# Kernel tuning notes

Hardware: AMD Instinct MI355X
Metric: run time of the kernel (lower is better)

The kernel has to match this reference:

```python
import jax, jax.numpy as jnp
import numpy as np

B, T, HID = 1, 2048, 1024
H, D = 16, 64
S = 64            # selection_block_size / sliding window / compress block
MAXK = 8          # max_selected_blocks
W_ENT, W_SP = 0.01, 0.01
NB = T // S       # 32 blocks (T divisible by S -> no padding branch)


def setup_inputs() -> dict:
    key = jax.random.key(0)
    ks = jax.random.split(key, 8)
    rn = lambda k, shp, s=0.02: jax.random.normal(k, shp, jnp.float32) * s
    return {
        'hidden_states': rn(ks[0], (B, T, HID), 1.0),
        'Wq': rn(ks[1], (HID, H * D)),
        'Wk': rn(ks[2], (HID, H * D)),
        'Wv': rn(ks[3], (HID, H * D)),
        'Wo': rn(ks[4], (H * D, HID)),
        'Wc': rn(ks[5], (S * D, D)),      # shared k/v compress MLP (same module in torch)
        'bc': jnp.zeros((D,), jnp.float32),
        'k_scale': jnp.ones((1,), jnp.float32),
        'k_bias': jnp.zeros((1,), jnp.float32),
        'Ws': rn(ks[6], (HID, 3 * H)),
        'bs': jnp.zeros((3 * H,), jnp.float32),
    }


def _local_attn(q, k, v):
    # lucidrains LocalAttention: window S, causal, look_backward=1, scale d^-0.5
    b, h, t, d = q.shape
    nw = t // S
    qw = q.reshape(b, h, nw, S, d)
    kw = k.reshape(b, h, nw, S, d)
    vw = v.reshape(b, h, nw, S, d)
    k_prev = jnp.concatenate([jnp.zeros_like(kw[:, :, :1]), kw[:, :, :-1]], axis=2)
    v_prev = jnp.concatenate([jnp.zeros_like(vw[:, :, :1]), vw[:, :, :-1]], axis=2)
    kc = jnp.concatenate([k_prev, kw], axis=3)   # (b,h,nw,2S,d)
    vc = jnp.concatenate([v_prev, vw], axis=3)
    scores = jnp.einsum('bhwid,bhwjd->bhwij', qw, kc) / jnp.sqrt(jnp.float32(d))
    qpos = jnp.arange(S)[:, None]
    krel = jnp.arange(2 * S)[None, :] - S        # key pos relative to window start
    wins = jnp.arange(nw)[:, None, None]
    allowed = (krel <= qpos)[None] & (wins * S + krel[None] >= 0)  # (nw,S,2S)
    NEG = -jnp.finfo(scores.dtype).max
    scores = jnp.where(allowed[None, None], scores, NEG)
    p = jax.nn.softmax(scores, axis=-1)
    return jnp.einsum('bhwij,bhwjd->bhwid', p, vc).reshape(b, h, t, d)


def reference(hidden_states, Wq, Wk, Wv, Wo, Wc, bc, k_scale, k_bias, Ws, bs):
    x = hidden_states
    scale = 1.0 / jnp.sqrt(jnp.float32(D))
    q = (x @ Wq).reshape(B, T, H, D).transpose(0, 2, 1, 3)
    k = (x @ Wk).reshape(B, T, H, D).transpose(0, 2, 1, 3)
    v = (x @ Wv).reshape(B, T, H, D).transpose(0, 2, 1, 3)

    sliding_out = _local_attn(q, k, v)

    # block compression (shared MLP for k and v, exact-erf GELU as in torch)
    k_blk = k.reshape(B, H, NB, S * D)
    v_blk = v.reshape(B, H, NB, S * D)
    kc = jax.nn.gelu(k_blk @ Wc + bc, approximate=False)   # (B,H,NB,D)
    vc = jax.nn.gelu(v_blk @ Wc + bc, approximate=False)

    importance = jnp.einsum('bhid,bhjd->bhij', q, kc) * scale   # (B,H,T,NB)
    comp_probs = jax.nn.softmax(importance, axis=-1)
    comp_out = jnp.einsum('bhij,bhjd->bhid', comp_probs, vc)

    # per-query-block scores, entropy-driven dynamic k
    block_scores = importance.reshape(B, H, NB, S, NB).mean(axis=3)   # (B,H,NB,NB)
    block_probs = jax.nn.softmax(block_scores, axis=-1)
    entropy = -jnp.sum(block_probs * jnp.log(block_probs + 1e-9), axis=-1)
    max_entropy = jnp.log(jnp.float32(NB))
    norm_ent = entropy / (max_entropy + 1e-9)
    k_ratio = jax.nn.sigmoid(k_scale[0] * norm_ent + k_bias[0])
    dynamic_k = jnp.clip(MAXK * k_ratio, 1.0, float(MAXK)).astype(jnp.int32)  # torch .long() truncates
    avg_k = dynamic_k.astype(jnp.float32).mean()

    _, topk_idx = jax.lax.top_k(block_scores, MAXK)                 # (B,H,NB,MAXK)
    k_mask = jnp.arange(MAXK)[None, None, None, :] < dynamic_k[..., None]
    sel = (topk_idx[..., None] == jnp.arange(NB)) & k_mask[..., None]
    mask = sel.any(axis=-2)                                         # (B,H,NB,NB)
    mask = mask | jnp.eye(NB, dtype=bool)[None, None]
    sparse_mask = jnp.repeat(jnp.repeat(mask, S, axis=2), S, axis=3)  # (B,H,T,T)

    attn = jnp.einsum('bhid,bhjd->bhij', q, k) * scale
    NEG = -jnp.finfo(attn.dtype).max
    attn = jnp.where(sparse_mask, attn, NEG)
    fine_probs = jax.nn.softmax(attn, axis=-1)
    fine_out = jnp.einsum('bhij,bhjd->bhid', fine_probs, v)

    strategy = jax.nn.sigmoid(x @ Ws + bs).reshape(B, T, H, 3).transpose(0, 2, 1, 3)  # (B,H,T,3)
    combined = jnp.stack([sliding_out, comp_out, fine_out], axis=-1)  # (B,H,T,D,3)
    out = jnp.einsum('bhnds,bhns->bhnd', combined, strategy)
    merged = out.transpose(0, 2, 1, 3).reshape(B, T, H * D)
    output = merged @ Wo

    entropy_loss = jnp.mean((k_ratio - norm_ent) ** 2)
    aux_loss = W_ENT * entropy_loss + W_SP * k_ratio.mean()
    return output, avg_k, aux_loss
```

## Files before the change

### kernel.cpp

```cpp
#include <hip/hip_runtime.h>
#include <math.h>
#include <stdint.h>

typedef unsigned short u16;
typedef short v8s __attribute__((ext_vector_type(8)));
typedef float v4f __attribute__((ext_vector_type(4)));

constexpr int kT   = 2048;
constexpr int kHID = 1024;
constexpr int kH   = 16;
constexpr int kNB  = 32;
constexpr size_t MB = 1ull << 20;

__device__ __forceinline__ float b2f(u16 u) { unsigned x = ((unsigned)u) << 16; return __uint_as_float(x); }
__device__ __forceinline__ u16 f2b(float f) {
  unsigned x = __float_as_uint(f);
  x += 0x7FFFu + ((x >> 16) & 1u);
  return (u16)(x >> 16);
}
__device__ __forceinline__ v4f mfma16(v8s a, v8s b, v4f c) {
  return __builtin_amdgcn_mfma_f32_16x16x32_bf16(a, b, c, 0, 0, 0);
}
__device__ __forceinline__ void gl_lds16(const void* g, void* l) {
  __builtin_amdgcn_global_load_lds((const __attribute__((address_space(1))) uint32_t*)g,
                                   (__attribute__((address_space(3))) uint32_t*)l, 16, 0, 0);
}

__global__ __launch_bounds__(256) void prep_kernel(
    const float* __restrict__ x, const float* __restrict__ Wq, const float* __restrict__ Wk,
    const float* __restrict__ Wv, const float* __restrict__ Wo, const float* __restrict__ Wc,
    const float* __restrict__ Wsp,
    u16* __restrict__ xh,
    u16* __restrict__ WqtH, u16* __restrict__ WktH,
    u16* __restrict__ WvtH, u16* __restrict__ WotH, u16* __restrict__ WctH, u16* __restrict__ WctL,
    u16* __restrict__ Wst) {
  __shared__ float tbuf[32][33];
  int bid = blockIdx.x;
  const int tid = threadIdx.x;
  if (bid < 1024) {
    int i = bid * 2048 + tid * 8;
    float4 a = *(const float4*)(x + i), b = *(const float4*)(x + i + 4);
    float tv[8] = {a.x, a.y, a.z, a.w, b.x, b.y, b.z, b.w};
    union { u16 s[8]; uint4 u; } hs;
#pragma unroll
    for (int e = 0; e < 8; ++e) hs.s[e] = f2b(tv[e]);
    *(uint4*)(xh + i) = hs.u;
    return;
  }
  bid -= 1024;
  const float* W; u16* Hh; u16* Ll; int Kd, Nd, bx, by;
  if (bid < 4096) {
    int wsel = bid >> 10, sub = bid & 1023;
    W  = wsel == 0 ? Wq : wsel == 1 ? Wk : wsel == 2 ? Wv : Wo;
    Hh = wsel == 0 ? WqtH : wsel == 1 ? WktH : wsel == 2 ? WvtH : WotH;
    Ll = nullptr;
    Kd = 1024; Nd = 1024;
    bx = (sub & 31) * 32; by = (sub >> 5) * 32;
  } else if (bid < 4096 + 256) {
    int sub = bid - 4096;
    W = Wc; Hh = WctH; Ll = WctL;
    Kd = 4096; Nd = 64;
    bx = (sub & 1) * 32; by = (sub >> 1) * 32;
  } else {
    int i = (bid - 4096 - 256) * 256 + tid;
    int n = i >> 10, k2 = i & 1023;
    float v = (n < 48) ? Wsp[(size_t)k2 * 48 + n] : 0.f;
    Wst[(size_t)n * 1024 + k2] = f2b(v);
    return;
  }
  const int lx = tid & 31, ly = tid >> 5;
  for (int i2 = ly; i2 < 32; i2 += 8) tbuf[i2][lx] = W[(size_t)(by + i2) * Nd + bx + lx];
  __syncthreads();
  for (int i2 = ly; i2 < 32; i2 += 8) {
    float xv = tbuf[lx][i2];
    size_t idx = (size_t)(bx + i2) * Kd + by + lx;
    u16 h = f2b(xv);
    Hh[idx] = h;
    if (Ll) Ll[idx] = f2b(xv - b2f(h));
  }
}

__global__ __launch_bounds__(256) void proj_gemm(const u16* __restrict__ xh,
                                                 const u16* __restrict__ WkH, const u16* __restrict__ WqH,
                                                 const u16* __restrict__ WvH, const u16* __restrict__ Wst,
                                                 const float* __restrict__ bsp,
                                                 u16* __restrict__ kbf, u16* __restrict__ qh,
                                                 u16* __restrict__ vbf, float* __restrict__ strat) {
  __shared__ u16 AsH[64 * 64], BsH[128 * 64];
  const int b = blockIdx.x;
  const int slot = (b & 7) * 100 + (b >> 3);
  const int panel = slot >> 5, bmi = slot & 31;
  int z, bni;
  if (panel < 8)       { z = 0; bni = panel; }
  else if (panel < 16) { z = 1; bni = panel - 8; }
  else if (panel < 24) { z = 2; bni = panel - 16; }
  else                 { z = 3; bni = 0; }
  const int bm = bmi * 64, bn = bni * 128;
  const u16* Bh = (z == 0) ? WkH : (z == 1) ? WqH : (z == 2) ? WvH : Wst;
  const int tid = threadIdx.x, w = tid >> 6, lane = tid & 63;
  const int lg = lane >> 4, l16 = lane & 15;
  const int wr = w >> 1, wc = w & 1;
  v4f acc[2][4] = {};
  for (int k0 = 0; k0 < kHID; k0 += 64) {
    __syncthreads();
#pragma unroll
    for (int p = 0; p < 2; ++p) {
      int s = tid + p * 256, row = s >> 3, sf = (s & 7) ^ (row & 7);
      gl_lds16(xh + (size_t)(bm + row) * kHID + k0 + sf * 8, (char*)AsH + s * 16);
    }
#pragma unroll
    for (int p = 0; p < 4; ++p) {
      int s = tid + p * 256, row = s >> 3, sf = (s & 7) ^ (row & 7);
      gl_lds16(Bh + (size_t)(bn + row) * kHID + k0 + sf * 8, (char*)BsH + s * 16);
    }
    __syncthreads();
#pragma unroll
    for (int kk = 0; kk < 2; ++kk) {
      v8s bh4[4];
#pragma unroll
      for (int j = 0; j < 4; ++j) {
        int col = wc * 64 + j * 16 + l16;
        bh4[j] = *(const v8s*)((const char*)BsH + col * 128 + (((kk * 4 + lg) ^ (col & 7)) * 16));
      }
#pragma unroll
      for (int i = 0; i < 2; ++i) {
        int row = wr * 32 + i * 16 + l16;
        v8s ah = *(const v8s*)((const char*)AsH + row * 128 + (((kk * 4 + lg) ^ (row & 7)) * 16));
#pragma unroll
        for (int j = 0; j < 4; ++j) acc[i][j] = mfma16(ah, bh4[j], acc[i][j]);
      }
    }
  }
#pragma unroll
  for (int i = 0; i < 2; ++i)
#pragma unroll
    for (int j = 0; j < 4; ++j)
#pragma unroll
      for (int r = 0; r < 4; ++r) {
        int row = bm + wr * 32 + i * 16 + lg * 4 + r;
        int col = bn + wc * 64 + j * 16 + l16;
        float val = acc[i][j][r];
        if (z == 3) {
          if (col < 48) strat[(size_t)row * 48 + col] = 1.f / (1.f + expf(-(val + bsp[col])));
        } else {
          u16 hh = f2b(val);
          size_t idx = (size_t)row * kHID + col;
          if (z == 0) kbf[idx] = hh;
          else if (z == 1) qh[idx] = hh;
          else vbf[idx] = hh;
        }
      }
}

__global__ __launch_bounds__(256) void cgemm_fused(const u16* __restrict__ kbf,
                                                   const u16* __restrict__ vbf,
                                                   const u16* __restrict__ WcH, const u16* __restrict__ WcL,
                                                   float* __restrict__ Pk, float* __restrict__ Pv) {
  __shared__ u16 AsH[64 * 64], BsH[64 * 64], BsL[64 * 64];
  const int bm = blockIdx.y * 64;
  const int isK = (blockIdx.z < 8);
  const int ks = isK ? blockIdx.z : blockIdx.z - 8;
  const u16* Asrc = isK ? kbf : vbf;
  float* P = isK ? Pk : Pv;
  const int tid = threadIdx.x;
  const int w = tid >> 6, lane = tid & 63;
  const int lg = lane >> 4, l16 = lane & 15;
  const int wr = w >> 1, wc = w & 1;
  v4f acc[2][2] = {};
  for (int k0 = ks * 512; k0 < ks * 512 + 512; k0 += 64) {
    __syncthreads();
#pragma unroll
    for (int ss = 0; ss < 2; ++ss) {
      int s = tid + ss * 256, row = s >> 3, sf = (s & 7) ^ (row & 7);
      int r = bm + row;
      size_t abase = ((size_t)((r & 31) * 64 + (k0 >> 6))) * kHID + (r >> 5) * 64 + sf * 8;
      gl_lds16(Asrc + abase, (char*)AsH + s * 16);
      gl_lds16(WcH + (size_t)row * 4096 + k0 + sf * 8, (char*)BsH + s * 16);
      if (isK) gl_lds16(WcL + (size_t)row * 4096 + k0 + sf * 8, (char*)BsL + s * 16);
    }
    __syncthreads();
    v8s ah[2][2], bh[2][2];
#pragma unroll
    for (int i = 0; i < 2; ++i)
#pragma unroll
      for (int kk = 0; kk < 2; ++kk) {
        int row = wr * 32 + i * 16 + l16;
        ah[i][kk] = *(const v8s*)((const char*)AsH + row * 128 + (((kk * 4 + lg) ^ (row & 7)) * 16));
        int col = wc * 32 + i * 16 + l16;
        bh[i][kk] = *(const v8s*)((const char*)BsH + col * 128 + (((kk * 4 + lg) ^ (col & 7)) * 16));
      }
#pragma unroll
    for (int i = 0; i < 2; ++i)
#pragma unroll
      for (int j = 0; j < 2; ++j) {
        acc[i][j] = mfma16(ah[i][0], bh[j][0], acc[i][j]);
        acc[i][j] = mfma16(ah[i][1], bh[j][1], acc[i][j]);
      }
    if (isK) {
      v8s bl[2][2];
#pragma unroll
      for (int i = 0; i < 2; ++i)
#pragma unroll
        for (int kk = 0; kk < 2; ++kk) {
          int col = wc * 32 + i * 16 + l16;
          bl[i][kk] = *(const v8s*)((const char*)BsL + col * 128 + (((kk * 4 + lg) ^ (col & 7)) * 16));
        }
#pragma unroll
      for (int i = 0; i < 2; ++i)
#pragma unroll
        for (int j = 0; j < 2; ++j) {
          acc[i][j] = mfma16(ah[i][0], bl[j][0], acc[i][j]);
          acc[i][j] = mfma16(ah[i][1], bl[j][1], acc[i][j]);
        }
    }
  }
#pragma unroll
  for (int i = 0; i < 2; ++i)
#pragma unroll
    for (int j = 0; j < 2; ++j)
#pragma unroll
      for (int r = 0; r < 4; ++r) {
        int row = bm + wr * 32 + i * 16 + lg * 4 + r;
        int col = wc * 32 + j * 16 + l16;
        P[(size_t)ks * 32768 + (size_t)row * 64 + col] = acc[i][j][r];
      }
}

__global__ __launch_bounds__(256) void impsel_mfma(const u16* __restrict__ qh,
                                                   const float* __restrict__ Pk,
                                                   const float* __restrict__ Pv,
                                                   const float* __restrict__ bc,
                                                   const float* __restrict__ strat,
                                                   const float* __restrict__ kscale_p,
                                                   const float* __restrict__ kbias_p,
                                                   unsigned* __restrict__ maskb,
                                                   float* __restrict__ krb,
                                                   float* __restrict__ neb,
                                                   int* __restrict__ dkb,
                                                   u16* __restrict__ merged) {
  __shared__ u16 KCH[32 * 64], KCL[32 * 64], VCT[64 * 32];
  __shared__ u16 Pl[4][16 * 32];
  __shared__ float red[4][32];
  const int tt = blockIdx.x, h = blockIdx.y;
  const int tid = threadIdx.x, w = tid >> 6, lane = tid & 63;
  const int lg = lane >> 4, l16 = lane & 15;
  {
    int nb = tid >> 3, seg = tid & 7;
    {
      const float* base = Pk + ((size_t)(h * 32 + nb) * 64 + seg * 8);
      float v[8] = {};
#pragma unroll
      for (int ks = 0; ks < 8; ++ks) {
        const float* p = base + (size_t)ks * 32768;
        float4 a = *(const float4*)p, bq = *(const float4*)(p + 4);
        v[0] += a.x; v[1] += a.y; v[2] += a.z; v[3] += a.w;
        v[4] += bq.x; v[5] += bq.y; v[6] += bq.z; v[7] += bq.w;
      }
      v8s hi, lo;
#pragma unroll
      for (int e = 0; e < 8; ++e) {
        float s = v[e] + bc[seg * 8 + e];
        float g = 0.5f * s * (1.f + erff(s * 0.70710678118654752f));
        u16 hh = f2b(g);
        hi[e] = (short)hh;
        lo[e] = (short)f2b(g - b2f(hh));
      }
      *(v8s*)((char*)KCH + nb * 128 + ((seg ^ (nb & 7)) * 16)) = hi;
      *(v8s*)((char*)KCL + nb * 128 + ((seg ^ (nb & 7)) * 16)) = lo;
    }
    {
      const float* base = Pv + ((size_t)(h * 32 + nb) * 64 + seg * 8);
      float v[8] = {};
#pragma unroll
      for (int ks = 0; ks < 8; ++ks) {
        const float* p = base + (size_t)ks * 32768;
        float4 a = *(const float4*)p, bq = *(const float4*)(p + 4);
        v[0] += a.x; v[1] += a.y; v[2] += a.z; v[3] += a.w;
        v[4] += bq.x; v[5] += bq.y; v[6] += bq.z; v[7] += bq.w;
      }
#pragma unroll
      for (int e = 0; e < 8; ++e) {
        int d = seg * 8 + e;
        float s = v[e] + bc[d];
        float g = 0.5f * s * (1.f + erff(s * 0.70710678118654752f));
        *((u16*)((char*)VCT + d * 64 + (((nb >> 3) ^ (d & 3)) * 16) + (nb & 7) * 2)) = f2b(g);
      }
    }
  }
  __syncthreads();
  const size_t qoff = (size_t)(tt * 64 + w * 16 + l16) * kHID + h * 64;
  v8s ah[2];
  ah[0] = *(const v8s*)(qh + qoff + lg * 8);
  ah[1] = *(const v8s*)(qh + qoff + 32 + lg * 8);
  v4f sa[2] = {};
#pragma unroll
  for (int ct = 0; ct < 2; ++ct) {
    int col = ct * 16 + l16;
#pragma unroll
    for (int kk = 0; kk < 2; ++kk) {
      int bo = col * 128 + (((kk * 4 + lg) ^ (col & 7)) * 16);
      v8s bh = *(const v8s*)((const char*)KCH + bo);
      v8s bl = *(const v8s*)((const char*)KCL + bo);
      sa[ct] = mfma16(ah[kk], bh, sa[ct]);
      sa[ct] = mfma16(ah[kk], bl, sa[ct]);
    }
  }
#pragma unroll
  for (int ct = 0; ct < 2; ++ct)
#pragma unroll
    for (int j = 0; j < 4; ++j) sa[ct][j] *= 0.125f;
#pragma unroll
  for (int ct = 0; ct < 2; ++ct) {
    float v = sa[ct][0] + sa[ct][1] + sa[ct][2] + sa[ct][3];
    v += __shfl_xor(v, 16, 64);
    v += __shfl_xor(v, 32, 64);
    if (lg == 0) red[w][ct * 16 + l16] = v;
  }
  float linv[4];
#pragma unroll
  for (int j = 0; j < 4; ++j) {
    float m = fmaxf(sa[0][j], sa[1][j]);
#pragma unroll
    for (int mm = 1; mm < 16; mm <<= 1) m = fmaxf(m, __shfl_xor(m, mm, 64));
    float e0 = __expf(sa[0][j] - m), e1 = __expf(sa[1][j] - m);
    float s = e0 + e1;
#pragma unroll
    for (int mm = 1; mm < 16; mm <<= 1) s += __shfl_xor(s, mm, 64);
    linv[j] = 1.f / s;
    int row = lg * 4 + j;
    Pl[w][row * 32 + l16] = f2b(e0);
    Pl[w][row * 32 + 16 + l16] = f2b(e1);
  }
  v8s pa = *(const v8s*)(&Pl[w][l16 * 32 + lg * 8]);
  v4f o[4] = {};
#pragma unroll
  for (int dt = 0; dt < 4; ++dt) {
    int d = dt * 16 + l16;
    v8s b = *(const v8s*)((const char*)VCT + d * 64 + ((lg ^ (d & 3)) * 16));
    o[dt] = mfma16(pa, b, o[dt]);
  }
#pragma unroll
  for (int dt = 0; dt < 4; ++dt)
#pragma unroll
    for (int j = 0; j < 4; ++j) {
      int t = tt * 64 + w * 16 + lg * 4 + j;
      int d = dt * 16 + l16;
      size_t mi = (size_t)t * kHID + h * 64 + d;
      merged[mi] = f2b(strat[t * 48 + h * 3 + 1] * (o[dt][j] * linv[j]));
    }
  __syncthreads();
  if (w == 0) {
    const int j = lane & 31;
    float bsj = (red[0][j] + red[1][j] + red[2][j] + red[3][j]) * (1.f / 64.f);
    float mx = bsj;
#pragma unroll
    for (int m = 1; m < 32; m <<= 1) mx = fmaxf(mx, __shfl_xor(mx, m, 64));
    float e = expf(bsj - mx);
    float lsum = e;
#pragma unroll
    for (int m = 1; m < 32; m <<= 1) lsum += __shfl_xor(lsum, m, 64);
    float p = e / lsum;
    float ent = p * logf(p + 1e-9f);
#pragma unroll
    for (int m = 1; m < 32; m <<= 1) ent += __shfl_xor(ent, m, 64);
    ent = -ent;
    float ne = ent / (logf(32.f) + 1e-9f);
    float kr = 1.f / (1.f + expf(-(kscale_p[0] * ne + kbias_p[0])));
    int dk = (int)fminf(fmaxf(8.f * kr, 1.f), 8.f);
    unsigned mword = 1u << tt;
    int taken = 0;
    for (int r = 0; r < dk; ++r) {
      float v2 = taken ? -3.4e38f : bsj;
      int idx2 = j;
#pragma unroll
      for (int m = 1; m < 32; m <<= 1) {
        float ov = __shfl_xor(v2, m, 64);
        int oi = __shfl_xor(idx2, m, 64);
        if (ov > v2 || (ov == v2 && oi < idx2)) { v2 = ov; idx2 = oi; }
      }
      mword |= (1u << idx2);
      if (j == idx2) taken = 1;
    }
    if (lane == 0) {
      maskb[h * kNB + tt] = mword;
      krb[h * kNB + tt] = kr;
      neb[h * kNB + tt] = ne;
      dkb[h * kNB + tt] = dk;
    }
  }
}

__global__ __launch_bounds__(256) void fineslide_mfma(const u16* __restrict__ qh,
                                                      const u16* __restrict__ kb_,
                                                      const u16* __restrict__ vb_,
                                                      const float* __restrict__ strat,
                                                      const unsigned* __restrict__ maskb,
                                                      const float* __restrict__ krb,
                                                      const float* __restrict__ neb,
                                                      const int* __restrict__ dkb,
                                                      float* __restrict__ outp,
                                                      u16* __restrict__ merged) {
  __shared__ u16 Kb[2][64 * 64];
  __shared__ u16 Vt[2][64 * 64];
  __shared__ u16 Pl[4][16 * 64];
  const int b = blockIdx.x;
  const int xcd = b & 7, slot = b >> 3;
  const int h = xcd + 8 * (slot >> 5);
  const int qb = slot & 31;
  const unsigned mword = maskb[h * kNB + qb];
  unsigned uni = mword | (1u << qb);
  if (qb > 0) uni |= 1u << (qb - 1);
  const int tid = threadIdx.x, w = tid >> 6, lane = tid & 63;
  const int lg = lane >> 4, l16 = lane & 15;
  if (b == 0 && w == 0) {
    float s1 = 0.f, s2 = 0.f, s3 = 0.f;
    for (int i = lane; i < 512; i += 64) {
      float fdk = (float)dkb[i], kr = krb[i], ne = neb[i];
      float d2 = kr - ne;
      s1 += fdk; s2 += d2 * d2; s3 += kr;
    }
#pragma unroll
    for (int m = 1; m < 64; m <<= 1) {
      s1 += __shfl_xor(s1, m, 64);
      s2 += __shfl_xor(s2, m, 64);
      s3 += __shfl_xor(s3, m, 64);
    }
    if (lane == 0) {
      outp[(size_t)kT * kHID + 0] = s1 * (1.f / 512.f);
      outp[(size_t)kT * kHID + 1] = 0.01f * (s2 * (1.f / 512.f)) + 0.01f * (s3 * (1.f / 512.f));
    }
  }
  v8s aq[2];
  {
    const u16* qrow = qh + (size_t)(qb * 64 + w * 16 + l16) * kHID + h * 64;
    aq[0] = *(const v8s*)(qrow + lg * 8);
    aq[1] = *(const v8s*)(qrow + 32 + lg * 8);
  }
  float mF[4], lF[4], mS[4], lS[4];
  v4f oF[4] = {}, oS[4] = {};
#pragma unroll
  for (int j = 0; j < 4; ++j) { mF[j] = -1e30f; lF[j] = 0.f; mS[j] = -1e30f; lS[j] = 0.f; }

  const int vkey = tid & 63, vd0 = (tid >> 6) * 16;

  auto k_stage = [&](int buf, int jb) {
#pragma unroll
    for (int ss = 0; ss < 2; ++ss) {
      int s = tid + ss * 256;
      int key = s >> 3, sf = (s & 7) ^ (key & 7);
      gl_lds16(kb_ + (size_t)(jb * 64 + key) * kHID + h * 64 + sf * 8, (char*)Kb[buf] + s * 16);
    }
  };
  auto v_issue = [&](int jb, uint4& c0, uint4& c1) {
    const u16* vsrc = vb_ + (size_t)(jb * 64 + vkey) * kHID + h * 64 + vd0;
    c0 = *(const uint4*)(vsrc);
    c1 = *(const uint4*)(vsrc + 8);
  };
  auto v_write = [&](int buf, uint4 c0, uint4 c1) {
    union { uint4 u[2]; u16 s[16]; } c;
    c.u[0] = c0; c.u[1] = c1;
#pragma unroll
    for (int i = 0; i < 16; ++i) {
      int d = vd0 + i;
      *((u16*)((char*)Vt[buf] + d * 128 + (((vkey >> 3) ^ (d & 7)) * 16)) + (vkey & 7)) = c.s[i];
    }
  };

  auto upd = [&](const v4f* sa, float* m_run, float* l_run, v4f* o_acc, int buf) {
    float corr[4];
#pragma unroll
    for (int j = 0; j < 4; ++j) {
      float t = fmaxf(fmaxf(sa[0][j], sa[1][j]), fmaxf(sa[2][j], sa[3][j]));
#pragma unroll
      for (int mm = 1; mm < 16; mm <<= 1) t = fmaxf(t, __shfl_xor(t, mm, 64));
      float mn = fmaxf(m_run[j], t);
      corr[j] = __expf(m_run[j] - mn);
      m_run[j] = mn;
    }
    float rs[4] = {0.f, 0.f, 0.f, 0.f};
    float pv[4][4];
#pragma unroll
    for (int ct = 0; ct < 4; ++ct)
#pragma unroll
      for (int j = 0; j < 4; ++j) {
        float e = __expf(sa[ct][j] - m_run[j]);
        pv[ct][j] = e;
        rs[j] += e;
      }
#pragma unroll
    for (int j = 0; j < 4; ++j) {
#pragma unroll
      for (int mm = 1; mm < 16; mm <<= 1) rs[j] += __shfl_xor(rs[j], mm, 64);
      l_run[j] = l_run[j] * corr[j] + rs[j];
    }
#pragma unroll
    for (int ct = 0; ct < 4; ++ct)
#pragma unroll
      for (int j = 0; j < 4; ++j) {
        int row = lg * 4 + j;
        int seg = ct * 2 + (l16 >> 3);
        *((u16*)((char*)Pl + w * 2048 + row * 128 + ((seg ^ (row & 7)) * 16)) + (l16 & 7)) = f2b(pv[ct][j]);
      }
#pragma unroll
    for (int dt = 0; dt < 4; ++dt)
#pragma unroll
      for (int j = 0; j < 4; ++j) o_acc[dt][j] *= corr[j];
#pragma unroll
    for (int dt = 0; dt < 4; ++dt) {
      int d = dt * 16 + l16;
#pragma unroll
      for (int kk = 0; kk < 2; ++kk) {
        v8s pa = *(const v8s*)((const char*)Pl + w * 2048 + l16 * 128 + (((kk * 4 + lg) ^ (l16 & 7)) * 16));
        v8s vb2 = *(const v8s*)((const char*)Vt[buf] + d * 128 + (((kk * 4 + lg) ^ (d & 7)) * 16));
        o_acc[dt] = mfma16(pa, vb2, o_acc[dt]);
      }
    }
  };

  int jb_cur = __builtin_ctz(uni);
  unsigned rem = uni & (uni - 1);
  uint4 vc0, vc1;
  v_issue(jb_cur, vc0, vc1);
  k_stage(0, jb_cur);
  v_write(0, vc0, vc1);
  int buf = 0;
  while (jb_cur >= 0) {
    int jb_next = -1;
    if (rem) { jb_next = __builtin_ctz(rem); rem &= rem - 1; }
    __syncthreads();
    if (jb_next >= 0) { v_issue(jb_next, vc0, vc1); k_stage(buf ^ 1, jb_next); }
    v4f sa[4] = {};
#pragma unroll
    for (int ct = 0; ct < 4; ++ct) {
      int key = ct * 16 + l16;
#pragma unroll
      for (int kk = 0; kk < 2; ++kk) {
        v8s bk = *(const v8s*)((const char*)Kb[buf] + key * 128 + (((kk * 4 + lg) ^ (key & 7)) * 16));
        sa[ct] = mfma16(aq[kk], bk, sa[ct]);
      }
    }
#pragma unroll
    for (int ct = 0; ct < 4; ++ct)
#pragma unroll
      for (int j = 0; j < 4; ++j) sa[ct][j] *= 0.125f;
    const bool inF = (mword >> jb_cur) & 1u;
    const bool inS = (jb_cur == qb) || (jb_cur + 1 == qb);
    if (inF) upd(sa, mF, lF, oF, buf);
    if (inS) {
      v4f sb[4];
#pragma unroll
      for (int ct = 0; ct < 4; ++ct) sb[ct] = sa[ct];
      if (jb_cur == qb) {
#pragma unroll
        for (int ct = 0; ct < 4; ++ct) {
          int key = ct * 16 + l16;
#pragma unroll
          for (int j = 0; j < 4; ++j) {
            int qp = w * 16 + lg * 4 + j;
            if (key > qp) sb[ct][j] = -1e30f;
          }
        }
      }
      upd(sb, mS, lS, oS, buf);
    }
    if (jb_next >= 0) v_write(buf ^ 1, vc0, vc1);
    jb_cur = jb_next;
    buf ^= 1;
  }
#pragma unroll
  for (int dt = 0; dt < 4; ++dt)
#pragma unroll
    for (int j = 0; j < 4; ++j) {
      int row = lg * 4 + j;
      int t = qb * 64 + w * 16 + row;
      int d = dt * 16 + l16;
      size_t idx = (size_t)t * kHID + h * 64 + d;
      float add = strat[t * 48 + h * 3 + 0] * (oS[dt][j] / lS[j]) +
                  strat[t * 48 + h * 3 + 2] * (oF[dt][j] / lF[j]);
      merged[idx] = f2b(b2f(merged[idx]) + add);
    }
}

__global__ __launch_bounds__(256) void gemm_out(const u16* __restrict__ A, const u16* __restrict__ Bt,
                                                float* __restrict__ Cf) {
  __shared__ u16 As[64 * 64], Bs[64 * 64];
  const int b = blockIdx.x;
  const int g = (b & 7) * 64 + (b >> 3);
  const int bn = (g >> 5) * 64;
  const int bm = (g & 31) * 64;
  const int tid = threadIdx.x, w = tid >> 6, lane = tid & 63;
  const int lg = lane >> 4, l16 = lane & 15;
  v4f acc[4] = {};
  for (int k0 = 0; k0 < kHID; k0 += 64) {
    __syncthreads();
#pragma unroll
    for (int p = 0; p < 2; ++p) {
      int s = tid + p * 256, row = s >> 3, sf = (s & 7) ^ (row & 7);
      gl_lds16(A + (size_t)(bm + row) * kHID + k0 + sf * 8, (char*)As + s * 16);
      gl_lds16(Bt + (size_t)(bn + row) * kHID + k0 + sf * 8, (char*)Bs + s * 16);
    }
    __syncthreads();
#pragma unroll
    for (int kk = 0; kk < 2; ++kk) {
      int row = w * 16 + l16;
      v8s a = *(const v8s*)((const char*)As + row * 128 + (((kk * 4 + lg) ^ (row & 7)) * 16));
#pragma unroll
      for (int j = 0; j < 4; ++j) {
        int col = j * 16 + l16;
        v8s bb = *(const v8s*)((const char*)Bs + col * 128 + (((kk * 4 + lg) ^ (col & 7)) * 16));
        acc[j] = mfma16(a, bb, acc[j]);
      }
    }
  }
#pragma unroll
  for (int j = 0; j < 4; ++j)
#pragma unroll
    for (int r = 0; r < 4; ++r) {
      int row = bm + w * 16 + lg * 4 + r;
      int col = bn + j * 16 + l16;
      Cf[(size_t)row * kHID + col] = acc[j][r];
    }
}

extern "C" void kernel_launch(void* const* d_in, const int* in_sizes, int n_in,
                              void* d_out, int out_size, void* d_ws, size_t ws_size,
                              hipStream_t stream) {
  const float* x      = (const float*)d_in[0];
  const float* Wq     = (const float*)d_in[1];
  const float* Wk     = (const float*)d_in[2];
  const float* Wv     = (const float*)d_in[3];
  const float* Wo     = (const float*)d_in[4];
  const float* Wc     = (const float*)d_in[5];
  const float* bc     = (const float*)d_in[6];
  const float* kscale = (const float*)d_in[7];
  const float* kbias  = (const float*)d_in[8];
  const float* Wsp    = (const float*)d_in[9];
  const float* bsp    = (const float*)d_in[10];
  float* out = (float*)d_out;
  char* W = (char*)d_ws;

  u16* qh     = (u16*)(W + 0 * MB);
  u16* kbf    = (u16*)(W + 8 * MB);
  u16* vbf    = (u16*)(W + 16 * MB);
  u16* merged = (u16*)(W + 20 * MB);
  u16* xh     = (u16*)(W + 24 * MB);
  u16* WqtH   = (u16*)(W + 32 * MB);
  u16* WktH   = (u16*)(W + 36 * MB);
  u16* WvtH   = (u16*)(W + 40 * MB);
  u16* WotH   = (u16*)(W + 42 * MB);
  u16* WctH   = (u16*)(W + 44 * MB);
  u16* WctL   = (u16*)(W + 44 * MB + 512 * 1024);
  u16* Wst    = (u16*)(W + 45 * MB);
  float* strat= (float*)(W + 46 * MB);
  float* Pk   = (float*)(W + 47 * MB);
  float* Pv   = (float*)(W + 48 * MB);
  unsigned* maskb = (unsigned*)(W + 49 * MB);
  float* krb  = (float*)(W + 49 * MB + 4 * 1024);
  float* neb  = (float*)(W + 49 * MB + 8 * 1024);
  int*   dkb  = (int*)(W + 49 * MB + 12 * 1024);

  dim3 b256(256);
  prep_kernel<<<5888, b256, 0, stream>>>(x, Wq, Wk, Wv, Wo, Wc, Wsp,
                                         xh, WqtH, WktH, WvtH, WotH, WctH, WctL, Wst);
  proj_gemm<<<800, b256, 0, stream>>>(xh, WktH, WqtH, WvtH, Wst,
                                      bsp, kbf, qh, vbf, strat);
  cgemm_fused<<<dim3(1, 8, 16), b256, 0, stream>>>(kbf, vbf, WctH, WctL, Pk, Pv);
  impsel_mfma<<<dim3(32, kH), b256, 0, stream>>>(qh, Pk, Pv, bc, strat,
                                                 kscale, kbias, maskb, krb, neb, dkb, merged);
  fineslide_mfma<<<512, b256, 0, stream>>>(qh, kbf, vbf, strat, maskb,
                                           krb, neb, dkb, out, merged);
  gemm_out<<<512, b256, 0, stream>>>(merged, WotH, out);
}
```

Before: 93.91 us.

## Fuse importance-selection kernel into fine/sliding attention kernel

Merges the compressed-attention and block-selection kernel into the fine/sliding attention kernel, so each (head, query-block) workgroup computes its selection mask locally and shares it through LDS instead of a global buffer. The merged output is written once instead of being written and then read-modify-written. The aux-loss reduction moves into the output GEMM kernel. This removes one launch plus the global round trips for the mask and the merged values, at the cost of a larger shared-memory footprint and a longer kernel.

```diff
diff --git a/kernel.cpp b/kernel.cpp
--- a/kernel.cpp
+++ b/kernel.cpp
@@ -226,24 +226,33 @@
       }
 }
 
-__global__ __launch_bounds__(256) void impsel_mfma(const u16* __restrict__ qh,
-                                                   const float* __restrict__ Pk,
-                                                   const float* __restrict__ Pv,
-                                                   const float* __restrict__ bc,
-                                                   const float* __restrict__ strat,
-                                                   const float* __restrict__ kscale_p,
-                                                   const float* __restrict__ kbias_p,
-                                                   unsigned* __restrict__ maskb,
-                                                   float* __restrict__ krb,
-                                                   float* __restrict__ neb,
-                                                   int* __restrict__ dkb,
-                                                   u16* __restrict__ merged) {
-  __shared__ u16 KCH[32 * 64], KCL[32 * 64], VCT[64 * 32];
-  __shared__ u16 Pl[4][16 * 32];
-  __shared__ float red[4][32];
-  const int tt = blockIdx.x, h = blockIdx.y;
+__global__ __launch_bounds__(256) void attn_fused(const u16* __restrict__ qh,
+                                                  const u16* __restrict__ kb_,
+                                                  const u16* __restrict__ vb_,
+                                                  const float* __restrict__ Pk,
+                                                  const float* __restrict__ Pv,
+                                                  const float* __restrict__ bc,
+                                                  const float* __restrict__ strat,
+                                                  const float* __restrict__ kscale_p,
+                                                  const float* __restrict__ kbias_p,
+                                                  float* __restrict__ krb,
+                                                  float* __restrict__ neb,
+                                                  int* __restrict__ dkb,
+                                                  u16* __restrict__ merged) {
+  __shared__ char smem[40960] __attribute__((aligned(128)));
+  const int b = blockIdx.x;
+  const int xcd = b & 7, slot = b >> 3;
+  const int h = xcd + 8 * (slot >> 5);
+  const int qb = slot & 31;
   const int tid = threadIdx.x, w = tid >> 6, lane = tid & 63;
   const int lg = lane >> 4, l16 = lane & 15;
+
+  char* KCH = smem;
+  char* KCL = smem + 4096;
+  char* VCT = smem + 8192;
+  u16*  PlA = (u16*)(smem + 12288);
+  float* red = (float*)(smem + 16384);
+  unsigned* mshare = (unsigned*)(smem + 16896);
   {
     int nb = tid >> 3, seg = tid & 7;
     {
@@ -265,8 +274,8 @@
         hi[e] = (short)hh;
         lo[e] = (short)f2b(g - b2f(hh));
       }
-      *(v8s*)((char*)KCH + nb * 128 + ((seg ^ (nb & 7)) * 16)) = hi;
-      *(v8s*)((char*)KCL + nb * 128 + ((seg ^ (nb & 7)) * 16)) = lo;
+      *(v8s*)(KCH + nb * 128 + ((seg ^ (nb & 7)) * 16)) = hi;
+      *(v8s*)(KCL + nb * 128 + ((seg ^ (nb & 7)) * 16)) = lo;
     }
     {
       const float* base = Pv + ((size_t)(h * 32 + nb) * 64 + seg * 8);
@@ -283,75 +292,72 @@
         int d = seg * 8 + e;
         float s = v[e] + bc[d];
         float g = 0.5f * s * (1.f + erff(s * 0.70710678118654752f));
-        *((u16*)((char*)VCT + d * 64 + (((nb >> 3) ^ (d & 3)) * 16) + (nb & 7) * 2)) = f2b(g);
+        *((u16*)(VCT + d * 64 + (((nb >> 3) ^ (d & 3)) * 16) + (nb & 7) * 2)) = f2b(g);
       }
     }
   }
   __syncthreads();
-  const size_t qoff = (size_t)(tt * 64 + w * 16 + l16) * kHID + h * 64;
-  v8s ah[2];
-  ah[0] = *(const v8s*)(qh + qoff + lg * 8);
-  ah[1] = *(const v8s*)(qh + qoff + 32 + lg * 8);
-  v4f sa[2] = {};
+  const size_t qoff = (size_t)(qb * 64 + w * 16 + l16) * kHID + h * 64;
+  v8s aq[2];
+  aq[0] = *(const v8s*)(qh + qoff + lg * 8);
+  aq[1] = *(const v8s*)(qh + qoff + 32 + lg * 8);
+  v4f sa2[2] = {};
 #pragma unroll
   for (int ct = 0; ct < 2; ++ct) {
     int col = ct * 16 + l16;
 #pragma unroll
     for (int kk = 0; kk < 2; ++kk) {
       int bo = col * 128 + (((kk * 4 + lg) ^ (col & 7)) * 16);
-      v8s bh = *(const v8s*)((const char*)KCH + bo);
-      v8s bl = *(const v8s*)((const char*)KCL + bo);
-      sa[ct] = mfma16(ah[kk], bh, sa[ct]);
-      sa[ct] = mfma16(ah[kk], bl, sa[ct]);
+      v8s bh = *(const v8s*)(KCH + bo);
+      v8s bl = *(const v8s*)(KCL + bo);
+      sa2[ct] = mfma16(aq[kk], bh, sa2[ct]);
+      sa2[ct] = mfma16(aq[kk], bl, sa2[ct]);
     }
   }
 #pragma unroll
   for (int ct = 0; ct < 2; ++ct)
 #pragma unroll
-    for (int j = 0; j < 4; ++j) sa[ct][j] *= 0.125f;
+    for (int j = 0; j < 4; ++j) sa2[ct][j] *= 0.125f;
 #pragma unroll
   for (int ct = 0; ct < 2; ++ct) {
-    float v = sa[ct][0] + sa[ct][1] + sa[ct][2] + sa[ct][3];
+    float v = sa2[ct][0] + sa2[ct][1] + sa2[ct][2] + sa2[ct][3];
     v += __shfl_xor(v, 16, 64);
     v += __shfl_xor(v, 32, 64);
-    if (lg == 0) red[w][ct * 16 + l16] = v;
+    if (lg == 0) red[w * 32 + ct * 16 + l16] = v;
   }
   float linv[4];
 #pragma unroll
   for (int j = 0; j < 4; ++j) {
-    float m = fmaxf(sa[0][j], sa[1][j]);
+    float m = fmaxf(sa2[0][j], sa2[1][j]);
 #pragma unroll
     for (int mm = 1; mm < 16; mm <<= 1) m = fmaxf(m, __shfl_xor(m, mm, 64));
-    float e0 = __expf(sa[0][j] - m), e1 = __expf(sa[1][j] - m);
+    float e0 = __expf(sa2[0][j] - m), e1 = __expf(sa2[1][j] - m);
     float s = e0 + e1;
 #pragma unroll
     for (int mm = 1; mm < 16; mm <<= 1) s += __shfl_xor(s, mm, 64);
     linv[j] = 1.f / s;
     int row = lg * 4 + j;
-    Pl[w][row * 32 + l16] = f2b(e0);
-    Pl[w][row * 32 + 16 + l16] = f2b(e1);
-  }
-  v8s pa = *(const v8s*)(&Pl[w][l16 * 32 + lg * 8]);
-  v4f o[4] = {};
-#pragma unroll
-  for (int dt = 0; dt < 4; ++dt) {
-    int d = dt * 16 + l16;
-    v8s b = *(const v8s*)((const char*)VCT + d * 64 + ((lg ^ (d & 3)) * 16));
-    o[dt] = mfma16(pa, b, o[dt]);
-  }
-#pragma unroll
-  for (int dt = 0; dt < 4; ++dt)
-#pragma unroll
-    for (int j = 0; j < 4; ++j) {
-      int t = tt * 64 + w * 16 + lg * 4 + j;
+    PlA[w * 512 + row * 32 + l16] = f2b(e0);
+    PlA[w * 512 + row * 32 + 16 + l16] = f2b(e1);
+  }
+  v8s pca = *(const v8s*)(PlA + w * 512 + l16 * 32 + lg * 8);
+  float compC[4][4];
+  {
+    v4f o[4];
+#pragma unroll
+    for (int dt = 0; dt < 4; ++dt) {
       int d = dt * 16 + l16;
-      size_t mi = (size_t)t * kHID + h * 64 + d;
-      merged[mi] = f2b(strat[t * 48 + h * 3 + 1] * (o[dt][j] * linv[j]));
-    }
+      v8s bb = *(const v8s*)(VCT + d * 64 + ((lg ^ (d & 3)) * 16));
+      v4f z = {};
+      o[dt] = mfma16(pca, bb, z);
+#pragma unroll
+      for (int j = 0; j < 4; ++j) compC[dt][j] = o[dt][j] * linv[j];
+    }
+  }
   __syncthreads();
   if (w == 0) {
     const int j = lane & 31;
-    float bsj = (red[0][j] + red[1][j] + red[2][j] + red[3][j]) * (1.f / 64.f);
+    float bsj = (red[j] + red[32 + j] + red[64 + j] + red[96 + j]) * (1.f / 64.f);
     float mx = bsj;
 #pragma unroll
     for (int m = 1; m < 32; m <<= 1) mx = fmaxf(mx, __shfl_xor(mx, m, 64));
@@ -367,7 +373,7 @@
     float ne = ent / (logf(32.f) + 1e-9f);
     float kr = 1.f / (1.f + expf(-(kscale_p[0] * ne + kbias_p[0])));
     int dk = (int)fminf(fmaxf(8.f * kr, 1.f), 8.f);
-    unsigned mword = 1u << tt;
+    unsigned mword = 1u << qb;
     int taken = 0;
     for (int r = 0; r < dk; ++r) {
       float v2 = taken ? -3.4e38f : bsj;
@@ -382,65 +388,25 @@
       if (j == idx2) taken = 1;
     }
     if (lane == 0) {
-      maskb[h * kNB + tt] = mword;
-      krb[h * kNB + tt] = kr;
-      neb[h * kNB + tt] = ne;
-      dkb[h * kNB + tt] = dk;
-    }
-  }
-}
-
-__global__ __launch_bounds__(256) void fineslide_mfma(const u16* __restrict__ qh,
-                                                      const u16* __restrict__ kb_,
-                                                      const u16* __restrict__ vb_,
-                                                      const float* __restrict__ strat,
-                                                      const unsigned* __restrict__ maskb,
-                                                      const float* __restrict__ krb,
-                                                      const float* __restrict__ neb,
-                                                      const int* __restrict__ dkb,
-                                                      float* __restrict__ outp,
-                                                      u16* __restrict__ merged) {
-  __shared__ u16 Kb[2][64 * 64];
-  __shared__ u16 Vt[2][64 * 64];
-  __shared__ u16 Pl[4][16 * 64];
-  const int b = blockIdx.x;
-  const int xcd = b & 7, slot = b >> 3;
-  const int h = xcd + 8 * (slot >> 5);
-  const int qb = slot & 31;
-  const unsigned mword = maskb[h * kNB + qb];
+      krb[h * kNB + qb] = kr;
+      neb[h * kNB + qb] = ne;
+      dkb[h * kNB + qb] = dk;
+      *mshare = mword;
+    }
+  }
+  __syncthreads();
+  const unsigned mword = *mshare;
+  __syncthreads();
+
+  char* KbB = smem;
+  char* VtB = smem + 16384;
+  char* PlB = smem + 32768;
   unsigned uni = mword | (1u << qb);
   if (qb > 0) uni |= 1u << (qb - 1);
-  const int tid = threadIdx.x, w = tid >> 6, lane = tid & 63;
-  const int lg = lane >> 4, l16 = lane & 15;
-  if (b == 0 && w == 0) {
-    float s1 = 0.f, s2 = 0.f, s3 = 0.f;
-    for (int i = lane; i < 512; i += 64) {
-      float fdk = (float)dkb[i], kr = krb[i], ne = neb[i];
-      float d2 = kr - ne;
-      s1 += fdk; s2 += d2 * d2; s3 += kr;
-    }
-#pragma unroll
-    for (int m = 1; m < 64; m <<= 1) {
-      s1 += __shfl_xor(s1, m, 64);
-      s2 += __shfl_xor(s2, m, 64);
-      s3 += __shfl_xor(s3, m, 64);
-    }
-    if (lane == 0) {
-      outp[(size_t)kT * kHID + 0] = s1 * (1.f / 512.f);
-      outp[(size_t)kT * kHID + 1] = 0.01f * (s2 * (1.f / 512.f)) + 0.01f * (s3 * (1.f / 512.f));
-    }
-  }
-  v8s aq[2];
-  {
-    const u16* qrow = qh + (size_t)(qb * 64 + w * 16 + l16) * kHID + h * 64;
-    aq[0] = *(const v8s*)(qrow + lg * 8);
-    aq[1] = *(const v8s*)(qrow + 32 + lg * 8);
-  }
   float mF[4], lF[4], mS[4], lS[4];
   v4f oF[4] = {}, oS[4] = {};
 #pragma unroll
   for (int j = 0; j < 4; ++j) { mF[j] = -1e30f; lF[j] = 0.f; mS[j] = -1e30f; lS[j] = 0.f; }
-
   const int vkey = tid & 63, vd0 = (tid >> 6) * 16;
 
   auto k_stage = [&](int buf, int jb) {
@@ -448,7 +414,7 @@
     for (int ss = 0; ss < 2; ++ss) {
       int s = tid + ss * 256;
       int key = s >> 3, sf = (s & 7) ^ (key & 7);
-      gl_lds16(kb_ + (size_t)(jb * 64 + key) * kHID + h * 64 + sf * 8, (char*)Kb[buf] + s * 16);
+      gl_lds16(kb_ + (size_t)(jb * 64 + key) * kHID + h * 64 + sf * 8, KbB + buf * 8192 + s * 16);
     }
   };
   auto v_issue = [&](int jb, uint4& c0, uint4& c1) {
@@ -462,10 +428,9 @@
 #pragma unroll
     for (int i = 0; i < 16; ++i) {
       int d = vd0 + i;
-      *((u16*)((char*)Vt[buf] + d * 128 + (((vkey >> 3) ^ (d & 7)) * 16)) + (vkey & 7)) = c.s[i];
+      *((u16*)(VtB + buf * 8192 + d * 128 + (((vkey >> 3) ^ (d & 7)) * 16)) + (vkey & 7)) = c.s[i];
     }
   };
-
   auto upd = [&](const v4f* sa, float* m_run, float* l_run, v4f* o_acc, int buf) {
     float corr[4];
 #pragma unroll
@@ -499,7 +464,7 @@
       for (int j = 0; j < 4; ++j) {
         int row = lg * 4 + j;
         int seg = ct * 2 + (l16 >> 3);
-        *((u16*)((char*)Pl + w * 2048 + row * 128 + ((seg ^ (row & 7)) * 16)) + (l16 & 7)) = f2b(pv[ct][j]);
+        *((u16*)(PlB + w * 2048 + row * 128 + ((seg ^ (row & 7)) * 16)) + (l16 & 7)) = f2b(pv[ct][j]);
       }
 #pragma unroll
     for (int dt = 0; dt < 4; ++dt)
@@ -510,8 +475,8 @@
       int d = dt * 16 + l16;
 #pragma unroll
       for (int kk = 0; kk < 2; ++kk) {
-        v8s pa = *(const v8s*)((const char*)Pl + w * 2048 + l16 * 128 + (((kk * 4 + lg) ^ (l16 & 7)) * 16));
-        v8s vb2 = *(const v8s*)((const char*)Vt[buf] + d * 128 + (((kk * 4 + lg) ^ (d & 7)) * 16));
+        v8s pa = *(const v8s*)(PlB + w * 2048 + l16 * 128 + (((kk * 4 + lg) ^ (l16 & 7)) * 16));
+        v8s vb2 = *(const v8s*)(VtB + buf * 8192 + d * 128 + (((kk * 4 + lg) ^ (d & 7)) * 16));
         o_acc[dt] = mfma16(pa, vb2, o_acc[dt]);
       }
     }
@@ -535,7 +500,7 @@
       int key = ct * 16 + l16;
 #pragma unroll
       for (int kk = 0; kk < 2; ++kk) {
-        v8s bk = *(const v8s*)((const char*)Kb[buf] + key * 128 + (((kk * 4 + lg) ^ (key & 7)) * 16));
+        v8s bk = *(const v8s*)(KbB + buf * 8192 + key * 128 + (((kk * 4 + lg) ^ (key & 7)) * 16));
         sa[ct] = mfma16(aq[kk], bk, sa[ct]);
       }
     }
@@ -568,21 +533,25 @@
     buf ^= 1;
   }
 #pragma unroll
-  for (int dt = 0; dt < 4; ++dt)
-#pragma unroll
-    for (int j = 0; j < 4; ++j) {
-      int row = lg * 4 + j;
-      int t = qb * 64 + w * 16 + row;
+  for (int j = 0; j < 4; ++j) {
+    int t = qb * 64 + w * 16 + lg * 4 + j;
+    float st0 = strat[t * 48 + h * 3 + 0];
+    float st1 = strat[t * 48 + h * 3 + 1];
+    float st2 = strat[t * 48 + h * 3 + 2];
+    float invS = 1.f / lS[j], invF = 1.f / lF[j];
+#pragma unroll
+    for (int dt = 0; dt < 4; ++dt) {
       int d = dt * 16 + l16;
       size_t idx = (size_t)t * kHID + h * 64 + d;
-      float add = strat[t * 48 + h * 3 + 0] * (oS[dt][j] / lS[j]) +
-                  strat[t * 48 + h * 3 + 2] * (oF[dt][j] / lF[j]);
-      merged[idx] = f2b(b2f(merged[idx]) + add);
-    }
+      float val = st0 * (oS[dt][j] * invS) + st1 * compC[dt][j] + st2 * (oF[dt][j] * invF);
+      merged[idx] = f2b(val);
+    }
+  }
 }
 
 __global__ __launch_bounds__(256) void gemm_out(const u16* __restrict__ A, const u16* __restrict__ Bt,
-                                                float* __restrict__ Cf) {
+                                                const float* __restrict__ krb, const float* __restrict__ neb,
+                                                const int* __restrict__ dkb, float* __restrict__ Cf) {
   __shared__ u16 As[64 * 64], Bs[64 * 64];
   const int b = blockIdx.x;
   const int g = (b & 7) * 64 + (b >> 3);
@@ -590,6 +559,24 @@
   const int bm = (g & 31) * 64;
   const int tid = threadIdx.x, w = tid >> 6, lane = tid & 63;
   const int lg = lane >> 4, l16 = lane & 15;
+  if (b == 0 && w == 3) {
+    float s1 = 0.f, s2 = 0.f, s3 = 0.f;
+    for (int i = lane; i < 512; i += 64) {
+      float fdk = (float)dkb[i], kr = krb[i], ne = neb[i];
+      float d2 = kr - ne;
+      s1 += fdk; s2 += d2 * d2; s3 += kr;
+    }
+#pragma unroll
+    for (int m = 1; m < 64; m <<= 1) {
+      s1 += __shfl_xor(s1, m, 64);
+      s2 += __shfl_xor(s2, m, 64);
+      s3 += __shfl_xor(s3, m, 64);
+    }
+    if (lane == 0) {
+      Cf[(size_t)kT * kHID + 0] = s1 * (1.f / 512.f);
+      Cf[(size_t)kT * kHID + 1] = 0.01f * (s2 * (1.f / 512.f)) + 0.01f * (s3 * (1.f / 512.f));
+    }
+  }
   v4f acc[4] = {};
   for (int k0 = 0; k0 < kHID; k0 += 64) {
     __syncthreads();
@@ -654,7 +641,6 @@
   float* strat= (float*)(W + 46 * MB);
   float* Pk   = (float*)(W + 47 * MB);
   float* Pv   = (float*)(W + 48 * MB);
-  unsigned* maskb = (unsigned*)(W + 49 * MB);
   float* krb  = (float*)(W + 49 * MB + 4 * 1024);
   float* neb  = (float*)(W + 49 * MB + 8 * 1024);
   int*   dkb  = (int*)(W + 49 * MB + 12 * 1024);
@@ -665,9 +651,7 @@
   proj_gemm<<<800, b256, 0, stream>>>(xh, WktH, WqtH, WvtH, Wst,
                                       bsp, kbf, qh, vbf, strat);
   cgemm_fused<<<dim3(1, 8, 16), b256, 0, stream>>>(kbf, vbf, WctH, WctL, Pk, Pv);
-  impsel_mfma<<<dim3(32, kH), b256, 0, stream>>>(qh, Pk, Pv, bc, strat,
-                                                 kscale, kbias, maskb, krb, neb, dkb, merged);
-  fineslide_mfma<<<512, b256, 0, stream>>>(qh, kbf, vbf, strat, maskb,
-                                           krb, neb, dkb, out, merged);
-  gemm_out<<<512, b256, 0, stream>>>(merged, WotH, out);
-}
+  attn_fused<<<512, b256, 0, stream>>>(qh, kbf, vbf, Pk, Pv, bc, strat,
+                                       kscale, kbias, krb, neb, dkb, merged);
+  gemm_out<<<512, b256, 0, stream>>>(merged, WotH, krb, neb, dkb, out);
+}
```

After: 88.87 us. 5.4% less time.
